# Kernel optimization log

Hardware: AMD Instinct MI355X
Metric: run time of the kernel (lower is better)

Reference implementation:

```python
import jax, jax.numpy as jnp
import numpy as np

DIM_NODE = 128
DIM_EDGE = 128
DIM_TIME = 100
NUM_HEAD = 8
DIM_OUT = 128
LN_EPS = 1e-5


def setup_inputs() -> dict:
    key = jax.random.key(0)
    ks = jax.random.split(key, 12)
    D, E = 25000, 250000
    src_feat = jax.random.normal(ks[0], (D + E, DIM_NODE), jnp.float32)
    edge_f = jax.random.normal(ks[1], (E, DIM_EDGE), jnp.float32)
    edge_dt = jax.random.uniform(ks[2], (E,), jnp.float32)
    src_idx = jnp.arange(D + E, dtype=jnp.int64)
    edge_dst = jnp.sort(jax.random.randint(ks[3], (E,), 0, D)).astype(jnp.int64)
    # TimeEncode params (fixed init from the module)
    time_w = jnp.asarray(1.0 / 10 ** np.linspace(0, 9, DIM_TIME, dtype=np.float32))  # (DIM_TIME,)
    time_b = jnp.zeros((DIM_TIME,), jnp.float32)
    dq = DIM_NODE + DIM_TIME           # 228
    dkv = DIM_NODE + DIM_EDGE + DIM_TIME  # 356
    s = 0.05
    wq_w = jax.random.normal(ks[4], (DIM_OUT, dq), jnp.float32) * s
    wq_b = jnp.zeros((DIM_OUT,), jnp.float32)
    wk_w = jax.random.normal(ks[5], (DIM_OUT, dkv), jnp.float32) * s
    wk_b = jnp.zeros((DIM_OUT,), jnp.float32)
    wv_w = jax.random.normal(ks[6], (DIM_OUT, dkv), jnp.float32) * s
    wv_b = jnp.zeros((DIM_OUT,), jnp.float32)
    wout_w = jax.random.normal(ks[7], (DIM_OUT, DIM_NODE + DIM_OUT), jnp.float32) * s
    wout_b = jnp.zeros((DIM_OUT,), jnp.float32)
    ln_g = jnp.ones((DIM_OUT,), jnp.float32)
    ln_b = jnp.zeros((DIM_OUT,), jnp.float32)
    return dict(src_feat=src_feat, edge_f=edge_f, edge_dt=edge_dt,
                time_w=time_w, time_b=time_b,
                wq_w=wq_w, wq_b=wq_b, wk_w=wk_w, wk_b=wk_b,
                wv_w=wv_w, wv_b=wv_b, wout_w=wout_w, wout_b=wout_b,
                ln_g=ln_g, ln_b=ln_b, src_idx=src_idx, edge_dst=edge_dst)


def reference(src_feat, edge_f, edge_dt, time_w, time_b,
              wq_w, wq_b, wk_w, wk_b, wv_w, wv_b,
              wout_w, wout_b, ln_g, ln_b, src_idx, edge_dst):
    E = edge_f.shape[0]
    src_data = src_feat[src_idx]              # (D+E, dn)
    D = src_data.shape[0] - E
    q_data = src_data[:D]                     # (D, dn)
    kv_data = src_data[D:]                    # (E, dn)

    # TimeEncode: cos(w * t + b)
    time_feat = jnp.cos(edge_dt[:, None] * time_w[None, :] + time_b)       # (E, dt)
    zero_time_feat = jnp.broadcast_to(jnp.cos(time_b), (D, DIM_TIME))      # (D, dt)

    Qd = jnp.concatenate([q_data, zero_time_feat], axis=1) @ wq_w.T + wq_b  # (D, dout)
    Q = Qd[edge_dst]                                                        # (E, dout)
    kv_in = jnp.concatenate([kv_data, edge_f, time_feat], axis=1)           # (E, dkv)
    K = kv_in @ wk_w.T + wk_b
    V = kv_in @ wv_w.T + wv_b

    dh = DIM_OUT // NUM_HEAD
    Q = Q.reshape(E, NUM_HEAD, dh)
    K = K.reshape(E, NUM_HEAD, dh)
    V = V.reshape(E, NUM_HEAD, dh)

    scores = jax.nn.leaky_relu(jnp.sum(Q * K, axis=2), 0.2)   # (E, H)
    # edge softmax: segment softmax over dst nodes
    m = jax.ops.segment_max(scores, edge_dst, num_segments=D)  # (D, H)
    m = jnp.where(jnp.isfinite(m), m, 0.0)
    ex = jnp.exp(scores - m[edge_dst])
    den = jax.ops.segment_sum(ex, edge_dst, num_segments=D)    # (D, H)
    att = ex / den[edge_dst]                                    # (E, H)

    Vw = (V * att[:, :, None]).reshape(E, DIM_OUT)
    h = jax.ops.segment_sum(Vw, edge_dst, num_segments=D)       # (D, dout)

    rst = jnp.concatenate([h, q_data], axis=1) @ wout_w.T + wout_b
    rst = jax.nn.relu(rst)
    mu = jnp.mean(rst, axis=-1, keepdims=True)
    var = jnp.var(rst, axis=-1, keepdims=True)
    return (rst - mu) / jnp.sqrt(var + LN_EPS) * ln_g + ln_b
```

## Files before the change

kernel.cpp:

```cpp
#include <hip/hip_runtime.h>
#include <stdint.h>

#define DIM_TIME 100
#define DQ 228
#define DKV 356
#define KPAD 384
#define NB 256
#define BM 64
#define BK 32
#define NCHUNK 12
#define A_STRIDE 392

typedef short v8s __attribute__((ext_vector_type(8)));
typedef float v4f __attribute__((ext_vector_type(4)));

__device__ __forceinline__ unsigned short bf16_bits(float f) {
    union { float f; uint32_t u; } c; c.f = f;
    uint32_t u = c.u;
    uint32_t r = (u + 0x7FFFu + ((u >> 16) & 1u)) >> 16;
    return (unsigned short)r;
}
__device__ __forceinline__ float bf16_to_f(unsigned short h) {
    union { uint32_t u; float f; } c; c.u = ((uint32_t)h) << 16; return c.f;
}

__global__ void prep_wt2(const float* __restrict__ wk_w, const float* __restrict__ wv_w,
                         unsigned short* __restrict__ Wt2) {
    int n = blockIdx.x;
    int k = threadIdx.x;
    float v = 0.f;
    if (k < DKV) v = (n < 128) ? wk_w[n * DKV + k] : wv_w[(n - 128) * DKV + k];
    Wt2[n * KPAD + k] = bf16_bits(v);
}

__global__ void prep_wqt(const float* __restrict__ wq_w, float* __restrict__ Wqt) {
    int k = blockIdx.x;
    int o = threadIdx.x;
    Wqt[k * 128 + o] = wq_w[o * DQ + k];
}

__global__ void prep_wot(const float* __restrict__ wout_w, float* __restrict__ Wot) {
    int k = blockIdx.x;
    int o = threadIdx.x;
    Wot[k * 128 + o] = wout_w[o * 256 + k];
}

__global__ void prep_cq(const float* __restrict__ wq_w, const float* __restrict__ wq_b,
                        const float* __restrict__ time_b, float* __restrict__ cq) {
    int o = threadIdx.x;
    float s = wq_b[o];
    for (int t = 0; t < DIM_TIME; ++t)
        s += cosf(time_b[t]) * wq_w[o * DQ + 128 + t];
    cq[o] = s;
}

__global__ __launch_bounds__(64) void qd_kernel(
        const float* __restrict__ src_feat, const int* __restrict__ src_idx,
        const float* __restrict__ Wqt, const float* __restrict__ cq,
        float* __restrict__ Qd, int D) {
    __shared__ float q_s[8][128];
    int o = threadIdx.x;
    int d0 = blockIdx.x * 8;
    #pragma unroll
    for (int i = 0; i < 8; ++i) {
        int d = d0 + i;
        float v0 = 0.f, v1 = 0.f;
        if (d < D) {
            const float* p = src_feat + (size_t)src_idx[d] * 128;
            v0 = p[o]; v1 = p[o + 64];
        }
        q_s[i][o] = v0; q_s[i][o + 64] = v1;
    }
    __syncthreads();
    float c0 = cq[o], c1 = cq[o + 64];
    float acc0[8], acc1[8];
    #pragma unroll
    for (int i = 0; i < 8; ++i) { acc0[i] = c0; acc1[i] = c1; }
    #pragma unroll 4
    for (int k = 0; k < 128; ++k) {
        float w0 = Wqt[k * 128 + o];
        float w1 = Wqt[k * 128 + 64 + o];
        #pragma unroll
        for (int i = 0; i < 8; ++i) {
            float a = q_s[i][k];
            acc0[i] += a * w0; acc1[i] += a * w1;
        }
    }
    #pragma unroll
    for (int i = 0; i < 8; ++i) {
        int d = d0 + i;
        if (d < D) {
            Qd[(size_t)d * 128 + o]      = acc0[i];
            Qd[(size_t)d * 128 + 64 + o] = acc1[i];
        }
    }
}

__global__ __launch_bounds__(256) void kv_mfma(
        const float* __restrict__ src_feat, const int* __restrict__ src_idx,
        const float* __restrict__ edge_f, const float* __restrict__ edge_dt,
        const float* __restrict__ time_w, const float* __restrict__ time_b,
        const unsigned short* __restrict__ Wt2,
        const float* __restrict__ wk_b, const float* __restrict__ wv_b,
        unsigned short* __restrict__ KVb, int D, int E) {
    __shared__ unsigned short A_s[BM * A_STRIDE];
    int tid = threadIdx.x;
    int e0 = blockIdx.x * BM;
    int lane = tid & 63;
    int wave = tid >> 6;
    int l15 = lane & 15, quad = lane >> 4;
    int wn = wave * 64;

    {
        int row = tid >> 2;
        int cb  = (tid & 3) * 8;
        int e = e0 + row;
        bool ok = (e < E);
        size_t nbase = ok ? (size_t)src_idx[D + e] * 128 : 0;
        #pragma unroll
        for (int i = 0; i < 8; ++i) {
            int c4 = cb + i;
            float4 v = ok ? *(const float4*)(src_feat + nbase + c4 * 4)
                          : make_float4(0.f, 0.f, 0.f, 0.f);
            ushort4 w;
            w.x = bf16_bits(v.x); w.y = bf16_bits(v.y);
            w.z = bf16_bits(v.z); w.w = bf16_bits(v.w);
            *(ushort4*)&A_s[row * A_STRIDE + c4 * 4] = w;
        }
        #pragma unroll
        for (int i = 0; i < 8; ++i) {
            int c4 = cb + i;
            float4 v = ok ? *(const float4*)(edge_f + (size_t)e * 128 + c4 * 4)
                          : make_float4(0.f, 0.f, 0.f, 0.f);
            ushort4 w;
            w.x = bf16_bits(v.x); w.y = bf16_bits(v.y);
            w.z = bf16_bits(v.z); w.w = bf16_bits(v.w);
            *(ushort4*)&A_s[row * A_STRIDE + 128 + c4 * 4] = w;
        }
    }
    {
        int c = tid & 127;
        int rbase = tid >> 7;
        bool vc = (c < DIM_TIME);
        float tw = vc ? time_w[c] : 0.f;
        float tb = vc ? time_b[c] : 0.f;
        #pragma unroll
        for (int i = 0; i < 32; ++i) {
            int row = i * 2 + rbase;
            int e = e0 + row;
            float v = 0.f;
            if (vc && e < E) v = __cosf(edge_dt[e] * tw + tb);
            A_s[row * A_STRIDE + 256 + c] = bf16_bits(v);
        }
    }
    __syncthreads();

    v4f acc[4][4];
    #pragma unroll
    for (int mf = 0; mf < 4; ++mf)
        #pragma unroll
        for (int nf = 0; nf < 4; ++nf)
            acc[mf][nf] = (v4f)(0.f);

    for (int ch = 0; ch < NCHUNK; ++ch) {
        v8s afrag[4], bfrag[4];
        #pragma unroll
        for (int nf = 0; nf < 4; ++nf)
            bfrag[nf] = *(const v8s*)(Wt2 + (size_t)(wn + nf * 16 + l15) * KPAD
                                      + ch * BK + quad * 8);
        #pragma unroll
        for (int mf = 0; mf < 4; ++mf)
            afrag[mf] = *(const v8s*)&A_s[(mf * 16 + l15) * A_STRIDE + ch * BK + quad * 8];
        #pragma unroll
        for (int mf = 0; mf < 4; ++mf)
            #pragma unroll
            for (int nf = 0; nf < 4; ++nf)
                acc[mf][nf] = __builtin_amdgcn_mfma_f32_16x16x32_bf16(
                                  afrag[mf], bfrag[nf], acc[mf][nf], 0, 0, 0);
    }

    #pragma unroll
    for (int nf = 0; nf < 4; ++nf) {
        int n = wn + nf * 16 + l15;
        float bias = (n < 128) ? wk_b[n] : wv_b[n - 128];
        #pragma unroll
        for (int mf = 0; mf < 4; ++mf) {
            #pragma unroll
            for (int r = 0; r < 4; ++r) {
                int e = e0 + mf * 16 + quad * 4 + r;
                if (e < E)
                    KVb[(size_t)e * NB + n] = bf16_bits(acc[mf][nf][r] + bias);
            }
        }
    }
}

__global__ void seg_offsets(const int* __restrict__ edge_dst, int* __restrict__ start,
                            int D, int E) {
    int d = blockIdx.x * blockDim.x + threadIdx.x;
    if (d > D) return;
    int lo = 0, hi = E;
    while (lo < hi) {
        int mid = (lo + hi) >> 1;
        if (edge_dst[mid] < d) lo = mid + 1; else hi = mid;
    }
    start[d] = lo;
}

__global__ __launch_bounds__(128) void attn_kernel(
        const float* __restrict__ Qd, const unsigned short* __restrict__ KVb,
        const int* __restrict__ start, float* __restrict__ h, int D) {
    int d = blockIdx.x;
    if (d >= D) return;
    int o = threadIdx.x;
    float q = Qd[(size_t)d * 128 + o];
    int s0 = start[d], s1 = start[d + 1];
    float m = -INFINITY, l = 0.f, acc = 0.f;
    for (int e = s0; e < s1; ++e) {
        float kf = bf16_to_f(KVb[(size_t)e * 256 + o]);
        float vf = bf16_to_f(KVb[(size_t)e * 256 + 128 + o]);
        float qk = q * kf;
        qk += __shfl_xor(qk, 8, 16);
        qk += __shfl_xor(qk, 4, 16);
        qk += __shfl_xor(qk, 2, 16);
        qk += __shfl_xor(qk, 1, 16);
        float s = qk > 0.f ? qk : 0.2f * qk;
        float nm = fmaxf(m, s);
        float sc = __expf(m - nm);
        float p  = __expf(s - nm);
        l   = l * sc + p;
        acc = acc * sc + p * vf;
        m = nm;
    }
    h[(size_t)d * 128 + o] = (l > 0.f) ? acc / l : 0.f;
}

__global__ __launch_bounds__(64) void out_kernel(
        const float* __restrict__ h, const float* __restrict__ src_feat,
        const int* __restrict__ src_idx, const float* __restrict__ Wot,
        const float* __restrict__ wout_b, const float* __restrict__ ln_g,
        const float* __restrict__ ln_b, float* __restrict__ out, int D) {
    __shared__ float in_s[8][256];
    int o = threadIdx.x;
    int d0 = blockIdx.x * 8;
    #pragma unroll
    for (int i = 0; i < 8; ++i) {
        int d = d0 + i;
        float a0 = 0.f, a1 = 0.f, b0 = 0.f, b1 = 0.f;
        if (d < D) {
            const float* ph = h + (size_t)d * 128;
            a0 = ph[o]; a1 = ph[o + 64];
            const float* pf = src_feat + (size_t)src_idx[d] * 128;
            b0 = pf[o]; b1 = pf[o + 64];
        }
        in_s[i][o] = a0; in_s[i][o + 64] = a1;
        in_s[i][128 + o] = b0; in_s[i][192 + o] = b1;
    }
    __syncthreads();
    float bb0 = wout_b[o], bb1 = wout_b[o + 64];
    float acc0[8], acc1[8];
    #pragma unroll
    for (int i = 0; i < 8; ++i) { acc0[i] = bb0; acc1[i] = bb1; }
    #pragma unroll 4
    for (int k = 0; k < 256; ++k) {
        float w0 = Wot[k * 128 + o];
        float w1 = Wot[k * 128 + 64 + o];
        #pragma unroll
        for (int i = 0; i < 8; ++i) {
            float a = in_s[i][k];
            acc0[i] += a * w0; acc1[i] += a * w1;
        }
    }
    float g0 = ln_g[o], g1 = ln_g[o + 64];
    float lb0 = ln_b[o], lb1 = ln_b[o + 64];
    #pragma unroll
    for (int i = 0; i < 8; ++i) {
        float v0 = fmaxf(acc0[i], 0.f), v1 = fmaxf(acc1[i], 0.f);
        float s1 = v0 + v1, s2 = v0 * v0 + v1 * v1;
        #pragma unroll
        for (int off = 32; off; off >>= 1) {
            s1 += __shfl_xor(s1, off);
            s2 += __shfl_xor(s2, off);
        }
        float mu  = s1 * (1.f / 128.f);
        float var = s2 * (1.f / 128.f) - mu * mu;
        float rs  = rsqrtf(var + 1e-5f);
        int d = d0 + i;
        if (d < D) {
            out[(size_t)d * 128 + o]      = (v0 - mu) * rs * g0 + lb0;
            out[(size_t)d * 128 + 64 + o] = (v1 - mu) * rs * g1 + lb1;
        }
    }
}

extern "C" void kernel_launch(void* const* d_in, const int* in_sizes, int n_in,
                              void* d_out, int out_size, void* d_ws, size_t ws_size,
                              hipStream_t stream) {
    const float* src_feat = (const float*)d_in[0];
    const float* edge_f   = (const float*)d_in[1];
    const float* edge_dt  = (const float*)d_in[2];
    const float* time_w   = (const float*)d_in[3];
    const float* time_b   = (const float*)d_in[4];
    const float* wq_w     = (const float*)d_in[5];
    const float* wq_b     = (const float*)d_in[6];
    const float* wk_w     = (const float*)d_in[7];
    const float* wk_b     = (const float*)d_in[8];
    const float* wv_w     = (const float*)d_in[9];
    const float* wv_b     = (const float*)d_in[10];
    const float* wout_w   = (const float*)d_in[11];
    const float* wout_b   = (const float*)d_in[12];
    const float* ln_g     = (const float*)d_in[13];
    const float* ln_b     = (const float*)d_in[14];
    const int*   src_idx  = (const int*)d_in[15];
    const int*   edge_dst = (const int*)d_in[16];

    int DE = in_sizes[0] / 128;
    int E  = in_sizes[1] / 128;
    int D  = DE - E;

    char* ws = (char*)d_ws;
    size_t off = 0;
    auto alloc = [&](size_t bytes) {
        void* p = ws + off;
        off = (off + bytes + 511) & ~(size_t)511;
        return p;
    };
    unsigned short* Wt2   = (unsigned short*)alloc((size_t)NB * KPAD * 2);
    float*          Wqt   = (float*)alloc(128 * 128 * 4);
    float*          Wot   = (float*)alloc(256 * 128 * 4);
    float*          cq    = (float*)alloc(128 * 4);
    float*          Qd    = (float*)alloc((size_t)D * 128 * 4);
    unsigned short* KVb   = (unsigned short*)alloc((size_t)E * 256 * 2);
    float*          hb    = (float*)alloc((size_t)D * 128 * 4);
    int*            start = (int*)alloc((size_t)(D + 1) * 4);

    hipLaunchKernelGGL(prep_wt2, dim3(NB), dim3(KPAD), 0, stream, wk_w, wv_w, Wt2);
    hipLaunchKernelGGL(prep_wqt, dim3(128), dim3(128), 0, stream, wq_w, Wqt);
    hipLaunchKernelGGL(prep_wot, dim3(256), dim3(128), 0, stream, wout_w, Wot);
    hipLaunchKernelGGL(prep_cq, dim3(1), dim3(128), 0, stream, wq_w, wq_b, time_b, cq);
    hipLaunchKernelGGL(qd_kernel, dim3((D + 7) / 8), dim3(64), 0, stream,
                       src_feat, src_idx, Wqt, cq, Qd, D);
    hipLaunchKernelGGL(kv_mfma, dim3((E + BM - 1) / BM), dim3(256), 0, stream,
                       src_feat, src_idx, edge_f, edge_dt, time_w, time_b,
                       Wt2, wk_b, wv_b, KVb, D, E);
    hipLaunchKernelGGL(seg_offsets, dim3((D + 1 + 255) / 256), dim3(256), 0, stream,
                       edge_dst, start, D, E);
    hipLaunchKernelGGL(attn_kernel, dim3(D), dim3(128), 0, stream, Qd, KVb, start, hb, D);
    hipLaunchKernelGGL(out_kernel, dim3((D + 7) / 8), dim3(64), 0, stream,
                       hb, src_feat, src_idx, Wot, wout_b, ln_g, ln_b, (float*)d_out, D);
}
```

Measured before the change: 648.7 us.

## Stage KV output through LDS, prefetch MFMA fragments, repack attention and GEMV blocks

Several kernels change at once. kv_mfma now double-buffers its A and B fragment loads across K chunks, and it writes K/V through shared memory so global stores are 16-byte coalesced rows instead of scattered 2-byte stores. attn_kernel now uses one wave per destination node and processes two channels per lane with 32-bit bf16 pair loads, replacing the 128-thread block per node. qd_kernel and out_kernel now pack four independent waves per block and drop the block barrier. These changes target store coalescing, load latency and launch granularity, at the cost of more registers and shared-memory reuse in kv_mfma.

```diff
diff --git a/kernel.cpp b/kernel.cpp
--- a/kernel.cpp
+++ b/kernel.cpp
@@ -10,6 +10,7 @@
 #define BK 32
 #define NCHUNK 12
 #define A_STRIDE 392
+#define C_STRIDE 264
 
 typedef short v8s __attribute__((ext_vector_type(8)));
 typedef float v4f __attribute__((ext_vector_type(4)));
@@ -20,8 +21,11 @@
     uint32_t r = (u + 0x7FFFu + ((u >> 16) & 1u)) >> 16;
     return (unsigned short)r;
 }
-__device__ __forceinline__ float bf16_to_f(unsigned short h) {
-    union { uint32_t u; float f; } c; c.u = ((uint32_t)h) << 16; return c.f;
+__device__ __forceinline__ float bf16_lo(uint32_t u) {
+    union { uint32_t u; float f; } c; c.u = u << 16; return c.f;
+}
+__device__ __forceinline__ float bf16_hi(uint32_t u) {
+    union { uint32_t u; float f; } c; c.u = u & 0xFFFF0000u; return c.f;
 }
 
 __global__ void prep_wt2(const float* __restrict__ wk_w, const float* __restrict__ wv_w,
@@ -34,14 +38,12 @@
 }
 
 __global__ void prep_wqt(const float* __restrict__ wq_w, float* __restrict__ Wqt) {
-    int k = blockIdx.x;
-    int o = threadIdx.x;
+    int k = blockIdx.x, o = threadIdx.x;
     Wqt[k * 128 + o] = wq_w[o * DQ + k];
 }
 
 __global__ void prep_wot(const float* __restrict__ wout_w, float* __restrict__ Wot) {
-    int k = blockIdx.x;
-    int o = threadIdx.x;
+    int k = blockIdx.x, o = threadIdx.x;
     Wot[k * 128 + o] = wout_w[o * 256 + k];
 }
 
@@ -54,35 +56,35 @@
     cq[o] = s;
 }
 
-__global__ __launch_bounds__(64) void qd_kernel(
+__global__ __launch_bounds__(256) void qd_kernel(
         const float* __restrict__ src_feat, const int* __restrict__ src_idx,
         const float* __restrict__ Wqt, const float* __restrict__ cq,
         float* __restrict__ Qd, int D) {
-    __shared__ float q_s[8][128];
-    int o = threadIdx.x;
-    int d0 = blockIdx.x * 8;
+    __shared__ float q_s[32][128];
+    int lane = threadIdx.x & 63, wave = threadIdx.x >> 6;
+    int r0 = wave * 8;
+    int d0 = blockIdx.x * 32 + r0;
     #pragma unroll
     for (int i = 0; i < 8; ++i) {
         int d = d0 + i;
         float v0 = 0.f, v1 = 0.f;
         if (d < D) {
             const float* p = src_feat + (size_t)src_idx[d] * 128;
-            v0 = p[o]; v1 = p[o + 64];
-        }
-        q_s[i][o] = v0; q_s[i][o + 64] = v1;
-    }
-    __syncthreads();
-    float c0 = cq[o], c1 = cq[o + 64];
+            v0 = p[lane]; v1 = p[lane + 64];
+        }
+        q_s[r0 + i][lane] = v0; q_s[r0 + i][lane + 64] = v1;
+    }
+    float c0 = cq[lane], c1 = cq[lane + 64];
     float acc0[8], acc1[8];
     #pragma unroll
     for (int i = 0; i < 8; ++i) { acc0[i] = c0; acc1[i] = c1; }
-    #pragma unroll 4
+    #pragma unroll 8
     for (int k = 0; k < 128; ++k) {
-        float w0 = Wqt[k * 128 + o];
-        float w1 = Wqt[k * 128 + 64 + o];
+        float w0 = Wqt[k * 128 + lane];
+        float w1 = Wqt[k * 128 + 64 + lane];
         #pragma unroll
         for (int i = 0; i < 8; ++i) {
-            float a = q_s[i][k];
+            float a = q_s[r0 + i][k];
             acc0[i] += a * w0; acc1[i] += a * w1;
         }
     }
@@ -90,8 +92,8 @@
     for (int i = 0; i < 8; ++i) {
         int d = d0 + i;
         if (d < D) {
-            Qd[(size_t)d * 128 + o]      = acc0[i];
-            Qd[(size_t)d * 128 + 64 + o] = acc1[i];
+            Qd[(size_t)d * 128 + lane]      = acc0[i];
+            Qd[(size_t)d * 128 + 64 + lane] = acc1[i];
         }
     }
 }
@@ -106,8 +108,7 @@
     __shared__ unsigned short A_s[BM * A_STRIDE];
     int tid = threadIdx.x;
     int e0 = blockIdx.x * BM;
-    int lane = tid & 63;
-    int wave = tid >> 6;
+    int lane = tid & 63, wave = tid >> 6;
     int l15 = lane & 15, quad = lane >> 4;
     int wn = wave * 64;
 
@@ -162,35 +163,56 @@
         for (int nf = 0; nf < 4; ++nf)
             acc[mf][nf] = (v4f)(0.f);
 
+    const unsigned short* wp = Wt2 + (size_t)(wn + l15) * KPAD + quad * 8;
+    const unsigned short* ap = A_s + l15 * A_STRIDE + quad * 8;
+
+    v8s bcur[4], acur[4];
+    #pragma unroll
+    for (int nf = 0; nf < 4; ++nf) bcur[nf] = *(const v8s*)(wp + nf * 16 * KPAD);
+    #pragma unroll
+    for (int mf = 0; mf < 4; ++mf) acur[mf] = *(const v8s*)(ap + mf * 16 * A_STRIDE);
+
+    #pragma unroll 2
     for (int ch = 0; ch < NCHUNK; ++ch) {
-        v8s afrag[4], bfrag[4];
-        #pragma unroll
-        for (int nf = 0; nf < 4; ++nf)
-            bfrag[nf] = *(const v8s*)(Wt2 + (size_t)(wn + nf * 16 + l15) * KPAD
-                                      + ch * BK + quad * 8);
-        #pragma unroll
-        for (int mf = 0; mf < 4; ++mf)
-            afrag[mf] = *(const v8s*)&A_s[(mf * 16 + l15) * A_STRIDE + ch * BK + quad * 8];
+        int k2 = (ch + 1 < NCHUNK) ? (ch + 1) * BK : 0;
+        v8s bn[4], an[4];
+        #pragma unroll
+        for (int nf = 0; nf < 4; ++nf) bn[nf] = *(const v8s*)(wp + nf * 16 * KPAD + k2);
+        #pragma unroll
+        for (int mf = 0; mf < 4; ++mf) an[mf] = *(const v8s*)(ap + mf * 16 * A_STRIDE + k2);
         #pragma unroll
         for (int mf = 0; mf < 4; ++mf)
             #pragma unroll
             for (int nf = 0; nf < 4; ++nf)
                 acc[mf][nf] = __builtin_amdgcn_mfma_f32_16x16x32_bf16(
-                                  afrag[mf], bfrag[nf], acc[mf][nf], 0, 0, 0);
-    }
-
+                                  acur[mf], bcur[nf], acc[mf][nf], 0, 0, 0);
+        #pragma unroll
+        for (int nf = 0; nf < 4; ++nf) bcur[nf] = bn[nf];
+        #pragma unroll
+        for (int mf = 0; mf < 4; ++mf) acur[mf] = an[mf];
+    }
+
+    __syncthreads();
     #pragma unroll
     for (int nf = 0; nf < 4; ++nf) {
         int n = wn + nf * 16 + l15;
         float bias = (n < 128) ? wk_b[n] : wv_b[n - 128];
         #pragma unroll
-        for (int mf = 0; mf < 4; ++mf) {
+        for (int mf = 0; mf < 4; ++mf)
             #pragma unroll
-            for (int r = 0; r < 4; ++r) {
-                int e = e0 + mf * 16 + quad * 4 + r;
-                if (e < E)
-                    KVb[(size_t)e * NB + n] = bf16_bits(acc[mf][nf][r] + bias);
-            }
+            for (int r = 0; r < 4; ++r)
+                A_s[(mf * 16 + quad * 4 + r) * C_STRIDE + n] =
+                    bf16_bits(acc[mf][nf][r] + bias);
+    }
+    __syncthreads();
+    #pragma unroll
+    for (int j = 0; j < 8; ++j) {
+        int c = j * 256 + tid;
+        int row = c >> 5;
+        int col = (c & 31) * 8;
+        if (e0 + row < E) {
+            v8s v = *(const v8s*)&A_s[row * C_STRIDE + col];
+            *(v8s*)&KVb[(size_t)(e0 + row) * NB + col] = v;
         }
     }
 }
@@ -207,72 +229,77 @@
     start[d] = lo;
 }
 
-__global__ __launch_bounds__(128) void attn_kernel(
+__global__ __launch_bounds__(256) void attn_kernel(
         const float* __restrict__ Qd, const unsigned short* __restrict__ KVb,
         const int* __restrict__ start, float* __restrict__ h, int D) {
-    int d = blockIdx.x;
-    if (d >= D) return;
-    int o = threadIdx.x;
-    float q = Qd[(size_t)d * 128 + o];
-    int s0 = start[d], s1 = start[d + 1];
-    float m = -INFINITY, l = 0.f, acc = 0.f;
-    for (int e = s0; e < s1; ++e) {
-        float kf = bf16_to_f(KVb[(size_t)e * 256 + o]);
-        float vf = bf16_to_f(KVb[(size_t)e * 256 + 128 + o]);
-        float qk = q * kf;
-        qk += __shfl_xor(qk, 8, 16);
-        qk += __shfl_xor(qk, 4, 16);
-        qk += __shfl_xor(qk, 2, 16);
-        qk += __shfl_xor(qk, 1, 16);
-        float s = qk > 0.f ? qk : 0.2f * qk;
-        float nm = fmaxf(m, s);
-        float sc = __expf(m - nm);
-        float p  = __expf(s - nm);
-        l   = l * sc + p;
-        acc = acc * sc + p * vf;
-        m = nm;
-    }
-    h[(size_t)d * 128 + o] = (l > 0.f) ? acc / l : 0.f;
-}
-
-__global__ __launch_bounds__(64) void out_kernel(
+    int lane = threadIdx.x & 63, wave = threadIdx.x >> 6;
+    int dbase = blockIdx.x * 16 + wave * 4;
+    for (int i = 0; i < 4; ++i) {
+        int d = dbase + i;
+        if (d >= D) break;
+        float2 q = *(const float2*)(Qd + (size_t)d * 128 + lane * 2);
+        int s0 = start[d], s1 = start[d + 1];
+        float m = -INFINITY, l = 0.f, a0 = 0.f, a1 = 0.f;
+        for (int e = s0; e < s1; ++e) {
+            const unsigned short* kv = KVb + (size_t)e * 256 + lane * 2;
+            uint32_t ku = *(const uint32_t*)kv;
+            uint32_t vu = *(const uint32_t*)(kv + 128);
+            float qk = q.x * bf16_lo(ku) + q.y * bf16_hi(ku);
+            qk += __shfl_xor(qk, 4, 8);
+            qk += __shfl_xor(qk, 2, 8);
+            qk += __shfl_xor(qk, 1, 8);
+            float s = qk > 0.f ? qk : 0.2f * qk;
+            float nm = fmaxf(m, s);
+            float sc = __expf(m - nm);
+            float p  = __expf(s - nm);
+            l  = l  * sc + p;
+            a0 = a0 * sc + p * bf16_lo(vu);
+            a1 = a1 * sc + p * bf16_hi(vu);
+            m = nm;
+        }
+        float inv = (l > 0.f) ? 1.f / l : 0.f;
+        *(float2*)(h + (size_t)d * 128 + lane * 2) = make_float2(a0 * inv, a1 * inv);
+    }
+}
+
+__global__ __launch_bounds__(256) void out_kernel(
         const float* __restrict__ h, const float* __restrict__ src_feat,
         const int* __restrict__ src_idx, const float* __restrict__ Wot,
         const float* __restrict__ wout_b, const float* __restrict__ ln_g,
         const float* __restrict__ ln_b, float* __restrict__ out, int D) {
-    __shared__ float in_s[8][256];
-    int o = threadIdx.x;
-    int d0 = blockIdx.x * 8;
+    __shared__ float in_s[32][256];
+    int lane = threadIdx.x & 63, wave = threadIdx.x >> 6;
+    int r0 = wave * 8;
+    int d0 = blockIdx.x * 32 + r0;
     #pragma unroll
     for (int i = 0; i < 8; ++i) {
         int d = d0 + i;
         float a0 = 0.f, a1 = 0.f, b0 = 0.f, b1 = 0.f;
         if (d < D) {
             const float* ph = h + (size_t)d * 128;
-            a0 = ph[o]; a1 = ph[o + 64];
+            a0 = ph[lane]; a1 = ph[lane + 64];
             const float* pf = src_feat + (size_t)src_idx[d] * 128;
-            b0 = pf[o]; b1 = pf[o + 64];
-        }
-        in_s[i][o] = a0; in_s[i][o + 64] = a1;
-        in_s[i][128 + o] = b0; in_s[i][192 + o] = b1;
-    }
-    __syncthreads();
-    float bb0 = wout_b[o], bb1 = wout_b[o + 64];
+            b0 = pf[lane]; b1 = pf[lane + 64];
+        }
+        in_s[r0 + i][lane] = a0; in_s[r0 + i][lane + 64] = a1;
+        in_s[r0 + i][128 + lane] = b0; in_s[r0 + i][192 + lane] = b1;
+    }
+    float bb0 = wout_b[lane], bb1 = wout_b[lane + 64];
     float acc0[8], acc1[8];
     #pragma unroll
     for (int i = 0; i < 8; ++i) { acc0[i] = bb0; acc1[i] = bb1; }
-    #pragma unroll 4
+    #pragma unroll 8
     for (int k = 0; k < 256; ++k) {
-        float w0 = Wot[k * 128 + o];
-        float w1 = Wot[k * 128 + 64 + o];
+        float w0 = Wot[k * 128 + lane];
+        float w1 = Wot[k * 128 + 64 + lane];
         #pragma unroll
         for (int i = 0; i < 8; ++i) {
-            float a = in_s[i][k];
+            float a = in_s[r0 + i][k];
             acc0[i] += a * w0; acc1[i] += a * w1;
         }
     }
-    float g0 = ln_g[o], g1 = ln_g[o + 64];
-    float lb0 = ln_b[o], lb1 = ln_b[o + 64];
+    float g0 = ln_g[lane], g1 = ln_g[lane + 64];
+    float lb0 = ln_b[lane], lb1 = ln_b[lane + 64];
     #pragma unroll
     for (int i = 0; i < 8; ++i) {
         float v0 = fmaxf(acc0[i], 0.f), v1 = fmaxf(acc1[i], 0.f);
@@ -287,8 +314,8 @@
         float rs  = rsqrtf(var + 1e-5f);
         int d = d0 + i;
         if (d < D) {
-            out[(size_t)d * 128 + o]      = (v0 - mu) * rs * g0 + lb0;
-            out[(size_t)d * 128 + 64 + o] = (v1 - mu) * rs * g1 + lb1;
+            out[(size_t)d * 128 + lane]      = (v0 - mu) * rs * g0 + lb0;
+            out[(size_t)d * 128 + 64 + lane] = (v1 - mu) * rs * g1 + lb1;
         }
     }
 }
@@ -338,14 +365,15 @@
     hipLaunchKernelGGL(prep_wqt, dim3(128), dim3(128), 0, stream, wq_w, Wqt);
     hipLaunchKernelGGL(prep_wot, dim3(256), dim3(128), 0, stream, wout_w, Wot);
     hipLaunchKernelGGL(prep_cq, dim3(1), dim3(128), 0, stream, wq_w, wq_b, time_b, cq);
-    hipLaunchKernelGGL(qd_kernel, dim3((D + 7) / 8), dim3(64), 0, stream,
+    hipLaunchKernelGGL(qd_kernel, dim3((D + 31) / 32), dim3(256), 0, stream,
                        src_feat, src_idx, Wqt, cq, Qd, D);
     hipLaunchKernelGGL(kv_mfma, dim3((E + BM - 1) / BM), dim3(256), 0, stream,
                        src_feat, src_idx, edge_f, edge_dt, time_w, time_b,
                        Wt2, wk_b, wv_b, KVb, D, E);
     hipLaunchKernelGGL(seg_offsets, dim3((D + 1 + 255) / 256), dim3(256), 0, stream,
                        edge_dst, start, D, E);
-    hipLaunchKernelGGL(attn_kernel, dim3(D), dim3(128), 0, stream, Qd, KVb, start, hb, D);
-    hipLaunchKernelGGL(out_kernel, dim3((D + 7) / 8), dim3(64), 0, stream,
+    hipLaunchKernelGGL(attn_kernel, dim3((D + 15) / 16), dim3(256), 0, stream,
+                       Qd, KVb, start, hb, D);
+    hipLaunchKernelGGL(out_kernel, dim3((D + 31) / 32), dim3(256), 0, stream,
                        hb, src_feat, src_idx, Wot, wout_b, ln_g, ln_b, (float*)d_out, D);
 }
```

Measured after the change: 640.0 us. No clear change (-1.3%).
